# Optimization experiments

Hardware: AMD Instinct MI355X
Metric: run time of the kernel (lower is better)

Reference implementation:

```python
import jax, jax.numpy as jnp
import numpy as np

# B=batch, T=time, H=hidden_size, D=vocos_dim, I=intermediate_dim, L=num_layers,
# CB=codebook_size, CD=codebook_dim (factorized VQ)
B, T, H, D, I, L, CB, CD = 8, 2048, 1024, 384, 2048, 12, 8192, 8


def _ln(h, g, b, eps=1e-6):
    # torch LayerNorm over last dim (biased variance)
    m = h.mean(-1, keepdims=True)
    v = h.var(-1, keepdims=True)
    return (h - m) / jnp.sqrt(v + eps) * g + b


def _conv1d(x, w, b, groups=1):
    # x: (B, Cin, T), w: (Cout, Cin//groups, 7), same-pad k=7
    y = jax.lax.conv_general_dilated(
        x, w, window_strides=(1,), padding=[(3, 3)],
        dimension_numbers=('NCH', 'OIH', 'NCH'), feature_group_count=groups)
    return y + b[None, :, None]


def setup_inputs() -> dict:
    key = jax.random.key(0)
    ks = iter(jax.random.split(key, 32))
    def nrm(shape):
        return jax.random.normal(next(ks), shape, jnp.float32) * 0.02
    d = {}
    d['x'] = jax.random.normal(next(ks), (B, T, H), jnp.float32)
    # VocosBackbone (encoder): embed conv + LN + 12 ConvNeXt blocks + final LN
    d['enc_embed_w'] = nrm((D, H, 7)); d['enc_embed_b'] = jnp.zeros((D,), jnp.float32)
    d['enc_norm_g'] = jnp.ones((D,), jnp.float32); d['enc_norm_b'] = jnp.zeros((D,), jnp.float32)
    d['enc_dw_w'] = nrm((L, D, 1, 7)); d['enc_dw_b'] = jnp.zeros((L, D), jnp.float32)
    d['enc_ln_g'] = jnp.ones((L, D), jnp.float32); d['enc_ln_b'] = jnp.zeros((L, D), jnp.float32)
    d['enc_w1'] = nrm((L, I, D)); d['enc_b1'] = jnp.zeros((L, I), jnp.float32)
    d['enc_w2'] = nrm((L, D, I)); d['enc_b2'] = jnp.zeros((L, D), jnp.float32)
    d['enc_gamma'] = jnp.full((L, D), 1.0 / L, jnp.float32)  # layer_scale init 1/num_layers
    d['enc_fnorm_g'] = jnp.ones((D,), jnp.float32); d['enc_fnorm_b'] = jnp.zeros((D,), jnp.float32)
    # nn.Linear(vocos_dim, hidden_size)
    d['enc_out_w'] = nrm((H, D)); d['enc_out_b'] = jnp.zeros((H,), jnp.float32)
    # Factorized ResidualVQ (single quantizer): 1024 -> 8, 8192-entry codebook, 8 -> 1024
    d['vq_in_w'] = nrm((CD, H)); d['vq_in_b'] = jnp.zeros((CD,), jnp.float32)
    d['codebook'] = jax.random.normal(next(ks), (CB, CD), jnp.float32)
    d['vq_out_w'] = nrm((H, CD)); d['vq_out_b'] = jnp.zeros((H,), jnp.float32)
    return d


def _encode(x, ew, eb, ng, nb, dww, dwb, lng, lnb, w1, b1, w2, b2, gamma, fg, fb, ow, ob):
    # x: (B, T, H) -> encoder output (B, T, H)
    h = _conv1d(x.transpose(0, 2, 1), ew, eb)            # (B, D, T)
    h = _ln(h.transpose(0, 2, 1), ng, nb)                # (B, T, D)
    for i in range(L):
        res = h
        y = _conv1d(h.transpose(0, 2, 1), dww[i], dwb[i], groups=D)  # depthwise (B, D, T)
        y = _ln(y.transpose(0, 2, 1), lng[i], lnb[i])                # (B, T, D)
        y = jax.nn.gelu(y @ w1[i].T + b1[i], approximate=False)       # (B, T, I)
        y = (y @ w2[i].T + b2[i]) * gamma[i]                          # (B, T, D)
        h = res + y
    h = _ln(h, fg, fb)
    return h @ ow.T + ob                                  # (B, T, H)


def _quantize(enc, in_w, in_b, codebook, out_w, out_b):
    z_e = enc @ in_w.T + in_b                             # (B, T, CD)
    z_n = z_e / jnp.maximum(jnp.linalg.norm(z_e, axis=-1, keepdims=True), 1e-12)
    cb_n = codebook / jnp.maximum(jnp.linalg.norm(codebook, axis=-1, keepdims=True), 1e-12)
    sim = jnp.einsum('btd,nd->btn', z_n, cb_n)            # cosine sim == argmin l2 on normalized vecs
    idx = jnp.argmax(sim, axis=-1)                        # (B, T) int
    z_q = codebook[idx]                                   # (B, T, CD) unnormalized codebook entries
    z_q = z_e + jax.lax.stop_gradient(z_q - z_e)          # straight-through estimator
    quantized = z_q @ out_w.T + out_b                     # (B, T, H)
    return idx, quantized


def reference(x, enc_embed_w, enc_embed_b, enc_norm_g, enc_norm_b, enc_dw_w, enc_dw_b,
              enc_ln_g, enc_ln_b, enc_w1, enc_b1, enc_w2, enc_b2, enc_gamma,
              enc_fnorm_g, enc_fnorm_b, enc_out_w, enc_out_b,
              vq_in_w, vq_in_b, codebook, vq_out_w, vq_out_b):
    enc = _encode(x, enc_embed_w, enc_embed_b, enc_norm_g, enc_norm_b, enc_dw_w, enc_dw_b,
                  enc_ln_g, enc_ln_b, enc_w1, enc_b1, enc_w2, enc_b2, enc_gamma,
                  enc_fnorm_g, enc_fnorm_b, enc_out_w, enc_out_b)
    idx, quantized = _quantize(enc, vq_in_w, vq_in_b, codebook, vq_out_w, vq_out_b)
    # RepCodec.quantize returns (indices (B,T), quantized_out.transpose(1,2) -> (B,T,H))
    return idx, quantized
```

## Files before the change

### kernel.cpp

```cpp
#include <hip/hip_runtime.h>
#include <math.h>


typedef _Float16 h8_t __attribute__((ext_vector_type(8)));
typedef _Float16 h4_t __attribute__((ext_vector_type(4)));
typedef float f4_t __attribute__((ext_vector_type(4)));

__device__ __forceinline__ float gelu_exact(float x){
  return 0.5f * x * (1.0f + erff(x * 0.70710678118654752f));
}

__device__ __forceinline__ void split4(const float4& a, h4_t& hi, h4_t& lo){
  float f[4] = {a.x,a.y,a.z,a.w};
  #pragma unroll
  for (int t=0;t<4;t++){
    _Float16 hh = (_Float16)f[t];
    hi[t] = hh;
    lo[t] = (_Float16)(f[t] - (float)hh);
  }
}

__device__ __forceinline__ int swz(int row, int kg){
  return row*32 + ((kg ^ ((row>>1)&3))<<3);
}

__device__ __forceinline__ void xcd_remap(int& bx, int& by){
  const int gx = gridDim.x;
  const int nwg = gx * gridDim.y;
  int bid = by*gx + bx;
  if ((nwg & 7) == 0){
    bid = (bid & 7)*(nwg >> 3) + (bid >> 3);
    bx = bid % gx; by = bid / gx;
  }
}


__global__ __launch_bounds__(256) void prep_wk_split(const float* __restrict__ w,
                                                     _Float16* __restrict__ wh,
                                                     _Float16* __restrict__ wl){
  int i = blockIdx.x*256 + threadIdx.x;
  if (i >= 384*1024) return;
  int d = i >> 10, c = i & 1023;
  #pragma unroll
  for (int k=0;k<7;k++){
    float v = w[(size_t)d*(1024*7) + (size_t)c*7 + k];
    _Float16 hh = (_Float16)v;
    wh[(size_t)k*393216 + i] = hh;
    wl[(size_t)k*393216 + i] = (_Float16)(v - (float)hh);
  }
}

__global__ __launch_bounds__(256) void prep_cb(const float* __restrict__ cb, float* __restrict__ cbn){
  int e = blockIdx.x*256 + threadIdx.x;
  if (e >= 8192) return;
  float v[8], s = 0.f;
  #pragma unroll
  for (int cd=0; cd<8; ++cd){ v[cd] = cb[(size_t)e*8+cd]; s += v[cd]*v[cd]; }
  float inv = 1.0f / fmaxf(sqrtf(s), 1e-12f);
  #pragma unroll
  for (int cd=0; cd<8; ++cd) cbn[(size_t)e*8+cd] = v[cd]*inv;
}

__global__ __launch_bounds__(256) void prep_cw(const float* __restrict__ viw, const float* __restrict__ ow,
                                               const float* __restrict__ vib, const float* __restrict__ ob,
                                               float* __restrict__ cw, float* __restrict__ cbias){
  int i = blockIdx.x*256 + threadIdx.x;
  if (i < 3072){
    int c = i / 384, d = i - c*384;
    float acc = 0.f;
    for (int h=0; h<1024; ++h)
      acc = fmaf(viw[c*1024+h], ow[(size_t)h*384 + d], acc);
    cw[i] = acc;
  }
  if (blockIdx.x == 0 && threadIdx.x < 8){
    int c = threadIdx.x;
    float acc = vib[c];
    for (int h=0; h<1024; ++h) acc = fmaf(viw[c*1024+h], ob[h], acc);
    cbias[c] = acc;
  }
}

__global__ __launch_bounds__(256) void split_pair(const float* __restrict__ a, const float* __restrict__ b,
                                                  _Float16* __restrict__ ah, _Float16* __restrict__ al,
                                                  _Float16* __restrict__ bh, _Float16* __restrict__ bl,
                                                  int n4){
  int i = blockIdx.x*256 + threadIdx.x;
  if (i >= n4) return;
  h4_t hi, lo;
  float4 va = ((const float4*)a)[i];
  split4(va, hi, lo);
  ((h4_t*)ah)[i] = hi; ((h4_t*)al)[i] = lo;
  float4 vb = ((const float4*)b)[i];
  split4(vb, hi, lo);
  ((h4_t*)bh)[i] = hi; ((h4_t*)bl)[i] = lo;
}

__global__ __launch_bounds__(256) void split_one(const float* __restrict__ a,
                                                 _Float16* __restrict__ ah, _Float16* __restrict__ al,
                                                 int n4){
  int i = blockIdx.x*256 + threadIdx.x;
  if (i >= n4) return;
  h4_t hi, lo;
  float4 va = ((const float4*)a)[i];
  split4(va, hi, lo);
  ((h4_t*)ah)[i] = hi; ((h4_t*)al)[i] = lo;
}

template<int BN, int EPI>
__global__ __launch_bounds__(256,2) void gemm_s(
    const _Float16* __restrict__ Ah, const _Float16* __restrict__ Al, int lda,
    const _Float16* __restrict__ Bh, const _Float16* __restrict__ Bl, int ldb,
    const float* __restrict__ bias,
    _Float16* __restrict__ Ch, _Float16* __restrict__ Cl,
    int ldc, int K)
{
  constexpr int NF = BN/32;
  __shared__ _Float16 AsH[4096], AsL[4096];
  __shared__ _Float16 BsH[BN*32], BsL[BN*32];
  const int tid = threadIdx.x;
  int bx = blockIdx.x, by = blockIdx.y;
  xcd_remap(bx, by);
  const int m0 = by*128, n0 = bx*BN;
  const int srow = tid>>2, kgs = tid&3, koff = kgs*8;
  const _Float16* pAh = Ah + (size_t)(m0+srow)*lda + koff;
  const _Float16* pAl = Al + (size_t)(m0+srow)*lda + koff;
  const _Float16* pBh = Bh + (size_t)(n0+srow)*ldb + koff;
  const _Float16* pBl = Bl + (size_t)(n0+srow)*ldb + koff;
  const int sA0 = swz(srow, kgs), sA1 = swz(srow+64, kgs);
  const int lane = tid & 63, wid = tid >> 6;
  const int wm = (wid>>1)*64, wn = (wid&1)*(BN/2);
  const int fr = lane & 15, kg = lane >> 4;
  f4_t acc[4][NF] = {};
  h8_t rah0 = *(const h8_t*)(pAh);
  h8_t rah1 = *(const h8_t*)(pAh + (size_t)64*lda);
  h8_t ral0 = *(const h8_t*)(pAl);
  h8_t ral1 = *(const h8_t*)(pAl + (size_t)64*lda);
  h8_t rbh0 = *(const h8_t*)(pBh);
  h8_t rbl0 = *(const h8_t*)(pBl);
  h8_t rbh1, rbl1;
  if constexpr (BN == 128){
    rbh1 = *(const h8_t*)(pBh + (size_t)64*ldb);
    rbl1 = *(const h8_t*)(pBl + (size_t)64*ldb);
  }
  for (int k0 = 0; k0 < K; k0 += 32){
    __syncthreads();
    *(h8_t*)(AsH + sA0) = rah0; *(h8_t*)(AsL + sA0) = ral0;
    *(h8_t*)(AsH + sA1) = rah1; *(h8_t*)(AsL + sA1) = ral1;
    *(h8_t*)(BsH + sA0) = rbh0; *(h8_t*)(BsL + sA0) = rbl0;
    if constexpr (BN == 128){
      *(h8_t*)(BsH + sA1) = rbh1; *(h8_t*)(BsL + sA1) = rbl1;
    }
    if (k0 + 32 < K){
      const int kn = k0 + 32;
      rah0 = *(const h8_t*)(pAh + kn);
      rah1 = *(const h8_t*)(pAh + (size_t)64*lda + kn);
      ral0 = *(const h8_t*)(pAl + kn);
      ral1 = *(const h8_t*)(pAl + (size_t)64*lda + kn);
      rbh0 = *(const h8_t*)(pBh + kn);
      rbl0 = *(const h8_t*)(pBl + kn);
      if constexpr (BN == 128){
        rbh1 = *(const h8_t*)(pBh + (size_t)64*ldb + kn);
        rbl1 = *(const h8_t*)(pBl + (size_t)64*ldb + kn);
      }
    }
    __syncthreads();
    h8_t ah[4], al[4], bh[NF], bl[NF];
    #pragma unroll
    for (int m=0;m<4;m++){
      int o = swz(wm + fr + m*16, kg);
      ah[m] = *(const h8_t*)(AsH + o);
      al[m] = *(const h8_t*)(AsL + o);
    }
    #pragma unroll
    for (int n=0;n<NF;n++){
      int o = swz(wn + fr + n*16, kg);
      bh[n] = *(const h8_t*)(BsH + o);
      bl[n] = *(const h8_t*)(BsL + o);
    }
    __builtin_amdgcn_s_setprio(1);
    #pragma unroll
    for (int m=0;m<4;m++)
      #pragma unroll
      for (int n=0;n<NF;n++){
        acc[m][n] = __builtin_amdgcn_mfma_f32_16x16x32_f16(al[m], bh[n], acc[m][n], 0,0,0);
        acc[m][n] = __builtin_amdgcn_mfma_f32_16x16x32_f16(ah[m], bl[n], acc[m][n], 0,0,0);
        acc[m][n] = __builtin_amdgcn_mfma_f32_16x16x32_f16(ah[m], bh[n], acc[m][n], 0,0,0);
      }
    __builtin_amdgcn_s_setprio(0);
  }
  float bj[NF];
  #pragma unroll
  for (int n=0;n<NF;n++) bj[n] = bias ? bias[n0 + wn + n*16 + fr] : 0.0f;
  #pragma unroll
  for (int m=0;m<4;m++){
    #pragma unroll
    for (int r=0;r<4;r++){
      const int row = m0 + wm + m*16 + kg*4 + r;
      #pragma unroll
      for (int n=0;n<NF;n++){
        const int col = n0 + wn + n*16 + fr;
        float v = acc[m][n][r] + bj[n];
        if (EPI==1) v = gelu_exact(v);
        _Float16 hh = (_Float16)v;
        Ch[(size_t)row*ldc + col] = hh;
        Cl[(size_t)row*ldc + col] = (_Float16)(v - (float)hh);
      }
    }
  }
}

__global__ __launch_bounds__(256,2) void gemm64(
    const _Float16* __restrict__ Ah, const _Float16* __restrict__ Al, int lda,
    const _Float16* __restrict__ Bh, const _Float16* __restrict__ Bl, int ldb,
    const float* __restrict__ bias, const float* __restrict__ gamma,
    float* __restrict__ C, int ldc, int K)
{
  __shared__ _Float16 AsH[8192], AsL[8192];
  __shared__ _Float16 BsH[4096], BsL[4096];
  const int tid = threadIdx.x;
  int bx = blockIdx.x, by = blockIdx.y;
  xcd_remap(bx, by);
  const int m0 = by*128, n0 = bx*64;
  const int srowA = tid>>1, khA = tid&1;
  const int srowB = tid>>2, kgB = tid&3;
  const _Float16* pAh = Ah + (size_t)(m0+srowA)*lda + khA*32;
  const _Float16* pAl = Al + (size_t)(m0+srowA)*lda + khA*32;
  const _Float16* pBh = Bh + (size_t)(n0+srowB)*ldb + kgB*8;
  const _Float16* pBl = Bl + (size_t)(n0+srowB)*ldb + kgB*8;
  const int lane = tid & 63, wid = tid >> 6;
  const int wm = (wid>>1)*64, wn = (wid&1)*32;
  const int fr = lane & 15, kg = lane >> 4;
  f4_t acc[4][2] = {};
  h8_t rAh[4], rAl[4], rBh[2], rBl[2];
  auto gload = [&](int k0){
    #pragma unroll
    for (int j=0;j<4;j++){
      rAh[j] = *(const h8_t*)(pAh + k0 + j*8);
      rAl[j] = *(const h8_t*)(pAl + k0 + j*8);
    }
    #pragma unroll
    for (int t=0;t<2;t++){
      rBh[t] = *(const h8_t*)(pBh + k0 + t*32);
      rBl[t] = *(const h8_t*)(pBl + k0 + t*32);
    }
  };
  gload(0);
  const int nt = K >> 6;
  for (int it = 0; it < nt; ++it){
    __syncthreads();
    #pragma unroll
    for (int j=0;j<4;j++){
      int slot = khA*4096 + swz(srowA, j);
      *(h8_t*)(AsH + slot) = rAh[j];
      *(h8_t*)(AsL + slot) = rAl[j];
    }
    #pragma unroll
    for (int t=0;t<2;t++){
      int slot = t*2048 + swz(srowB, kgB);
      *(h8_t*)(BsH + slot) = rBh[t];
      *(h8_t*)(BsL + slot) = rBl[t];
    }
    if (it + 1 < nt) gload((it+1) << 6);
    __syncthreads();
    #pragma unroll
    for (int s=0;s<2;s++){
      h8_t ah[4], al[4], bh[2], bl[2];
      #pragma unroll
      for (int m=0;m<4;m++){
        int o = s*4096 + swz(wm + fr + m*16, kg);
        ah[m] = *(const h8_t*)(AsH + o);
        al[m] = *(const h8_t*)(AsL + o);
      }
      #pragma unroll
      for (int n=0;n<2;n++){
        int o = s*2048 + swz(wn + fr + n*16, kg);
        bh[n] = *(const h8_t*)(BsH + o);
        bl[n] = *(const h8_t*)(BsL + o);
      }
      __builtin_amdgcn_s_setprio(1);
      #pragma unroll
      for (int m=0;m<4;m++)
        #pragma unroll
        for (int n=0;n<2;n++){
          acc[m][n] = __builtin_amdgcn_mfma_f32_16x16x32_f16(al[m], bh[n], acc[m][n], 0,0,0);
          acc[m][n] = __builtin_amdgcn_mfma_f32_16x16x32_f16(ah[m], bl[n], acc[m][n], 0,0,0);
          acc[m][n] = __builtin_amdgcn_mfma_f32_16x16x32_f16(ah[m], bh[n], acc[m][n], 0,0,0);
        }
      __builtin_amdgcn_s_setprio(0);
    }
  }
  float bj[2], gj[2];
  #pragma unroll
  for (int n=0;n<2;n++){
    int col = n0 + wn + n*16 + fr;
    bj[n] = bias ? bias[col] : 0.0f;
    gj[n] = gamma[col];
  }
  #pragma unroll
  for (int m=0;m<4;m++){
    #pragma unroll
    for (int r=0;r<4;r++){
      const int row = m0 + wm + m*16 + kg*4 + r;
      #pragma unroll
      for (int n=0;n<2;n++){
        const int col = n0 + wn + n*16 + fr;
        C[(size_t)row*ldc + col] += gj[n]*(acc[m][n][r] + bj[n]);
      }
    }
  }
}

__global__ __launch_bounds__(256,2) void embed_f16(
    const _Float16* __restrict__ xh, const _Float16* __restrict__ xl,
    const _Float16* __restrict__ wkh, const _Float16* __restrict__ wkl,
    const float* __restrict__ bias, float* __restrict__ C)
{
  __shared__ _Float16 AsH[8192], AsL[8192], BsH[4096], BsL[4096];
  const int tid = threadIdx.x;
  int bx = blockIdx.x, by = blockIdx.y;
  xcd_remap(bx, by);
  const int m0 = by*128, n0 = bx*64;
  const int srowA = tid>>1, khA = tid&1;
  const int srowB = tid>>2, kgB = tid&3;
  const int rA = m0 + srowA, tA = rA & 2047;
  const int lane = tid & 63, wid = tid >> 6;
  const int wm = (wid>>1)*64, wn = (wid&1)*32;
  const int fr = lane & 15, kg = lane >> 4;
  f4_t acc[4][2] = {};
  const h8_t zero8 = {0,0,0,0,0,0,0,0};
  h8_t rAh[4], rAl[4], rBh[2], rBl[2];
  auto load_tile = [&](int it){
    const int k = it >> 4;
    const int k0 = (it & 15) << 6;
    const bool v = (unsigned)(tA + k - 3) < 2048u;
    const _Float16* ph = xh + (size_t)(rA + k - 3)*1024 + k0 + khA*32;
    const _Float16* pl = xl + (size_t)(rA + k - 3)*1024 + k0 + khA*32;
    #pragma unroll
    for (int j=0;j<4;j++){
      rAh[j] = v ? *(const h8_t*)(ph + j*8) : zero8;
      rAl[j] = v ? *(const h8_t*)(pl + j*8) : zero8;
    }
    const _Float16* qh = wkh + (size_t)k*393216 + (size_t)(n0+srowB)*1024 + k0 + kgB*8;
    const _Float16* ql = wkl + (size_t)k*393216 + (size_t)(n0+srowB)*1024 + k0 + kgB*8;
    #pragma unroll
    for (int t=0;t<2;t++){
      rBh[t] = *(const h8_t*)(qh + t*32);
      rBl[t] = *(const h8_t*)(ql + t*32);
    }
  };
  load_tile(0);
  for (int it = 0; it < 112; ++it){
    __syncthreads();
    #pragma unroll
    for (int j=0;j<4;j++){
      int slot = khA*4096 + swz(srowA, j);
      *(h8_t*)(AsH + slot) = rAh[j];
      *(h8_t*)(AsL + slot) = rAl[j];
    }
    #pragma unroll
    for (int t=0;t<2;t++){
      int slot = t*2048 + swz(srowB, kgB);
      *(h8_t*)(BsH + slot) = rBh[t];
      *(h8_t*)(BsL + slot) = rBl[t];
    }
    if (it + 1 < 112) load_tile(it + 1);
    __syncthreads();
    #pragma unroll
    for (int s=0;s<2;s++){
      h8_t ah[4], al[4], bh[2], bl[2];
      #pragma unroll
      for (int m=0;m<4;m++){
        int o = s*4096 + swz(wm + fr + m*16, kg);
        ah[m] = *(const h8_t*)(AsH + o);
        al[m] = *(const h8_t*)(AsL + o);
      }
      #pragma unroll
      for (int n=0;n<2;n++){
        int o = s*2048 + swz(wn + fr + n*16, kg);
        bh[n] = *(const h8_t*)(BsH + o);
        bl[n] = *(const h8_t*)(BsL + o);
      }
      __builtin_amdgcn_s_setprio(1);
      #pragma unroll
      for (int m=0;m<4;m++)
        #pragma unroll
        for (int n=0;n<2;n++){
          acc[m][n] = __builtin_amdgcn_mfma_f32_16x16x32_f16(al[m], bh[n], acc[m][n], 0,0,0);
          acc[m][n] = __builtin_amdgcn_mfma_f32_16x16x32_f16(ah[m], bl[n], acc[m][n], 0,0,0);
          acc[m][n] = __builtin_amdgcn_mfma_f32_16x16x32_f16(ah[m], bh[n], acc[m][n], 0,0,0);
        }
      __builtin_amdgcn_s_setprio(0);
    }
  }
  #pragma unroll
  for (int m=0;m<4;m++){
    #pragma unroll
    for (int r=0;r<4;r++){
      const int row = m0 + wm + m*16 + kg*4 + r;
      #pragma unroll
      for (int n=0;n<2;n++){
        const int col = n0 + wn + n*16 + fr;
        C[(size_t)row*384 + col] = acc[m][n][r] + bias[col];
      }
    }
  }
}

template<bool CONV, bool SPLIT>
__global__ __launch_bounds__(384) void ln_kernel(
    const float* __restrict__ in,
    const float* __restrict__ dw, const float* __restrict__ db,
    const float* __restrict__ g, const float* __restrict__ b,
    float* __restrict__ out, _Float16* __restrict__ oh, _Float16* __restrict__ ol)
{
  __shared__ float rs[6], rs2[6], stat[2];
  const int m = blockIdx.x, d = threadIdx.x;
  float v;
  if (CONV){
    const int t = m & 2047;
    float a = db[d];
    #pragma unroll
    for (int k=0;k<7;k++){
      int tt = t + k - 3;
      if ((unsigned)tt < 2048u) a = fmaf(in[(size_t)(m + k - 3)*384 + d], dw[d*7 + k], a);
    }
    v = a;
  } else {
    v = in[(size_t)m*384 + d];
  }
  float s = v, s2 = v*v;
  #pragma unroll
  for (int o=1;o<64;o<<=1){ s += __shfl_xor(s,o); s2 += __shfl_xor(s2,o); }
  const int wid = d >> 6, lane = d & 63;
  if (lane == 0){ rs[wid]=s; rs2[wid]=s2; }
  __syncthreads();
  if (d == 0){
    float S=0.f, S2=0.f;
    #pragma unroll
    for (int w=0;w<6;w++){ S+=rs[w]; S2+=rs2[w]; }
    float mean = S*(1.0f/384.0f);
    float var = fmaxf(S2*(1.0f/384.0f) - mean*mean, 0.0f);
    stat[0]=mean; stat[1]=1.0f/sqrtf(var + 1e-6f);
  }
  __syncthreads();
  float o = (v - stat[0])*stat[1]*g[d] + b[d];
  if (SPLIT){
    _Float16 hh = (_Float16)o;
    oh[(size_t)m*384 + d] = hh;
    ol[(size_t)m*384 + d] = (_Float16)(o - (float)hh);
  } else {
    out[(size_t)m*384 + d] = o;
  }
}


__global__ __launch_bounds__(256) void vq_ze(
    const float* __restrict__ y, const float* __restrict__ cw,
    const float* __restrict__ cbias, float* __restrict__ zn)
{
  __shared__ float scw[3072];
  const int tid = threadIdx.x;
  for (int i = tid; i < 3072; i += 256) scw[i] = cw[i];
  __syncthreads();
  const int wid = tid >> 6, lane = tid & 63;
  const size_t m = (size_t)blockIdx.x*4 + wid;
  float acc[8] = {};
  #pragma unroll
  for (int j=0;j<6;j++){
    float v = y[m*384 + j*64 + lane];
    #pragma unroll
    for (int cd=0;cd<8;cd++) acc[cd] = fmaf(v, scw[cd*384 + j*64 + lane], acc[cd]);
  }
  #pragma unroll
  for (int cd=0;cd<8;cd++)
    #pragma unroll
    for (int o=1;o<64;o<<=1) acc[cd] += __shfl_xor(acc[cd], o);
  if (lane == 0){
    float z[8], s = 0.f;
    #pragma unroll
    for (int cd=0;cd<8;cd++){ z[cd] = acc[cd] + cbias[cd]; s += z[cd]*z[cd]; }
    float inv = 1.0f / fmaxf(sqrtf(s), 1e-12f);
    #pragma unroll
    for (int cd=0;cd<8;cd++) zn[m*8+cd] = z[cd]*inv;
  }
}

__global__ __launch_bounds__(256) void vq_argmax(
    const float* __restrict__ zn, const float* __restrict__ cbn,
    int* __restrict__ idx_out, float* __restrict__ idx_f)
{
  __shared__ float sbest[256];
  __shared__ int   sidx[256];
  const int tid = threadIdx.x;
  const int tok = tid & 31, ch = tid >> 5;
  const size_t m = (size_t)blockIdx.x*32 + tok;
  float4 z0 = *(const float4*)&zn[m*8];
  float4 z1 = *(const float4*)&zn[m*8+4];
  float best = -1e30f; int bidx = 0;
  const float* cp = cbn + (size_t)ch*8192;
  #pragma unroll 4
  for (int e = 0; e < 1024; ++e){
    const float4 ca  = *(const float4*)&cp[e*8];
    const float4 cb4 = *(const float4*)&cp[e*8+4];
    float s = z0.x*ca.x + z0.y*ca.y + z0.z*ca.z + z0.w*ca.w
            + z1.x*cb4.x + z1.y*cb4.y + z1.z*cb4.z + z1.w*cb4.w;
    if (s > best){ best = s; bidx = ch*1024 + e; }
  }
  sbest[tid] = best; sidx[tid] = bidx;
  __syncthreads();
  if (tid < 32){
    float b = sbest[tid]; int bi = sidx[tid];
    #pragma unroll
    for (int c=1;c<8;c++){
      float ob = sbest[c*32 + tid];
      if (ob > b){ b = ob; bi = sidx[c*32 + tid]; }
    }
    idx_out[(size_t)blockIdx.x*32 + tid] = bi;
    idx_f [(size_t)blockIdx.x*32 + tid] = (float)bi;
  }
}

__global__ __launch_bounds__(256) void vq_out_kernel(
    const int* __restrict__ idx, const float* __restrict__ cb,
    const float* __restrict__ wo, const float* __restrict__ bo,
    float* __restrict__ outq)
{
  __shared__ float wT[8][1024];
  __shared__ float cbs[16][8];
  __shared__ int idxs[16];
  const int tid = threadIdx.x;
  #pragma unroll
  for (int j=0;j<4;j++){
    int hcol = j*256 + tid;
    float4 w0 = *(const float4*)&wo[(size_t)hcol*8];
    float4 w1 = *(const float4*)&wo[(size_t)hcol*8+4];
    wT[0][hcol]=w0.x; wT[1][hcol]=w0.y; wT[2][hcol]=w0.z; wT[3][hcol]=w0.w;
    wT[4][hcol]=w1.x; wT[5][hcol]=w1.y; wT[6][hcol]=w1.z; wT[7][hcol]=w1.w;
  }
  if (tid < 16) idxs[tid] = idx[blockIdx.x*16 + tid];
  __syncthreads();
  if (tid < 128){ int tk = tid>>3, cd = tid&7; cbs[tk][cd] = cb[(size_t)idxs[tk]*8 + cd]; }
  __syncthreads();
  float bb[4];
  #pragma unroll
  for (int j=0;j<4;j++) bb[j] = bo[j*256+tid];
  for (int tk=0;tk<16;tk++){
    const size_t m = (size_t)blockIdx.x*16 + tk;
    float c0=cbs[tk][0], c1=cbs[tk][1], c2=cbs[tk][2], c3=cbs[tk][3];
    float c4=cbs[tk][4], c5=cbs[tk][5], c6=cbs[tk][6], c7=cbs[tk][7];
    #pragma unroll
    for (int j=0;j<4;j++){
      int hcol = j*256 + tid;
      float v = bb[j];
      v = fmaf(c0, wT[0][hcol], v); v = fmaf(c1, wT[1][hcol], v);
      v = fmaf(c2, wT[2][hcol], v); v = fmaf(c3, wT[3][hcol], v);
      v = fmaf(c4, wT[4][hcol], v); v = fmaf(c5, wT[5][hcol], v);
      v = fmaf(c6, wT[6][hcol], v); v = fmaf(c7, wT[7][hcol], v);
      outq[m*1024 + hcol] = v;
    }
  }
}


extern "C" void kernel_launch(void* const* d_in, const int* in_sizes, int n_in,
                              void* d_out, int out_size, void* d_ws, size_t ws_size,
                              hipStream_t stream) {
  (void)in_sizes; (void)n_in; (void)out_size; (void)ws_size;
  const float* x   = (const float*)d_in[0];
  const float* eww = (const float*)d_in[1];
  const float* ewb = (const float*)d_in[2];
  const float* ng  = (const float*)d_in[3];
  const float* nb  = (const float*)d_in[4];
  const float* dww = (const float*)d_in[5];
  const float* dwb = (const float*)d_in[6];
  const float* lng = (const float*)d_in[7];
  const float* lnb = (const float*)d_in[8];
  const float* w1  = (const float*)d_in[9];
  const float* b1  = (const float*)d_in[10];
  const float* w2  = (const float*)d_in[11];
  const float* b2  = (const float*)d_in[12];
  const float* gma = (const float*)d_in[13];
  const float* fg  = (const float*)d_in[14];
  const float* fb  = (const float*)d_in[15];
  const float* ow  = (const float*)d_in[16];
  const float* ob  = (const float*)d_in[17];
  const float* viw = (const float*)d_in[18];
  const float* vib = (const float*)d_in[19];
  const float* cb  = (const float*)d_in[20];
  const float* vow = (const float*)d_in[21];
  const float* vob = (const float*)d_in[22];
  float* out = (float*)d_out;

  float* ws = (float*)d_ws;
  float* wreg = ws;
  _Float16* wkh = (_Float16*)wreg;
  _Float16* wkl = wkh + 2752512;
  _Float16* w1h = (_Float16*)wreg;
  _Float16* w1l = w1h + 786432;
  _Float16* w2h = w1h + 1572864;
  _Float16* w2l = w1h + 2359296;
  float* zn  = wreg + 1048576;
  float* cbn = wreg + 1179648;
  int*  idxb = (int*)(wreg + 1245184);
  float* cw  = wreg + 1261568;
  float* cbias = wreg + 1264640;
  float* h   = ws + 2752512;
  float* ylreg = ws + 9043968;
  float* yf32 = ylreg;
  _Float16* ylh = (_Float16*)ylreg;
  _Float16* yll = ylh + 6291456;
  float* y1reg = ws + 15335424;
  _Float16* xh  = (_Float16*)y1reg;
  _Float16* xl  = xh + 16777216;
  _Float16* y1h = (_Float16*)y1reg;
  _Float16* y1l = y1h + 16777216;

  prep_wk_split<<<dim3(1536), dim3(256), 0, stream>>>(eww, wkh, wkl);
  split_one<<<dim3(16384), dim3(256), 0, stream>>>(x, xh, xl, 4194304);
  embed_f16<<<dim3(6,128), dim3(256), 0, stream>>>(xh, xl, wkh, wkl, ewb, yf32);
  ln_kernel<false,false><<<dim3(16384), dim3(384), 0, stream>>>(
      yf32, nullptr, nullptr, ng, nb, h, nullptr, nullptr);

  for (int i = 0; i < 12; ++i){
    split_pair<<<dim3(768), dim3(256), 0, stream>>>(
        w1 + (size_t)i*786432, w2 + (size_t)i*786432, w1h, w1l, w2h, w2l, 196608);
    ln_kernel<true,true><<<dim3(16384), dim3(384), 0, stream>>>(
        h, dww + (size_t)i*2688, dwb + (size_t)i*384,
        lng + (size_t)i*384, lnb + (size_t)i*384, nullptr, ylh, yll);
    for (int ic = 0; ic < 2; ++ic){
      gemm_s<128,1><<<dim3(8,128), dim3(256), 0, stream>>>(
          ylh, yll, 384,
          w1h + (size_t)ic*393216, w1l + (size_t)ic*393216, 384,
          b1 + (size_t)i*2048 + (size_t)ic*1024,
          y1h, y1l, 1024, 384);
      gemm64<<<dim3(6,128), dim3(256), 0, stream>>>(
          y1h, y1l, 1024,
          w2h + (size_t)ic*1024, w2l + (size_t)ic*1024, 2048,
          (ic == 0) ? (b2 + (size_t)i*384) : nullptr,
          gma + (size_t)i*384,
          h, 384, 1024);
    }
  }

  ln_kernel<false,false><<<dim3(16384), dim3(384), 0, stream>>>(
      h, nullptr, nullptr, fg, fb, yf32, nullptr, nullptr);
  prep_cw<<<dim3(12), dim3(256), 0, stream>>>(viw, ow, vib, ob, cw, cbias);
  prep_cb<<<dim3(32), dim3(256), 0, stream>>>(cb, cbn);
  vq_ze<<<dim3(4096), dim3(256), 0, stream>>>(yf32, cw, cbias, zn);
  vq_argmax<<<dim3(512), dim3(256), 0, stream>>>(zn, cbn, idxb, out);
  vq_out_kernel<<<dim3(1024), dim3(256), 0, stream>>>(idxb, cb, vow, vob, out + 16384);
}
```

Baseline: 3.761 ms.

## Use 256x128 tiles with 32x32 MFMA for FFN up-projection, shrink K-tile elsewhere

The first FFN GEMM (w1 plus GELU) now uses 256x128 block tiles and 32x32x16 MFMA instructions, so fewer blocks each reuse more data per LDS load. The down-projection and embed-conv GEMMs drop from a 64-wide K step to a 32-wide K step, which halves their LDS footprint to allow higher occupancy but doubles the number of barrier-separated iterations. The larger w1 tile raises register and LDS pressure, and the B-tile store in gemm_n64 needs a conditional offset for rows beyond 64.

```diff
diff --git a/kernel.cpp b/kernel.cpp
--- a/kernel.cpp
+++ b/kernel.cpp
@@ -5,6 +5,7 @@
 typedef _Float16 h8_t __attribute__((ext_vector_type(8)));
 typedef _Float16 h4_t __attribute__((ext_vector_type(4)));
 typedef float f4_t __attribute__((ext_vector_type(4)));
+typedef float f32x16 __attribute__((ext_vector_type(16)));
 
 __device__ __forceinline__ float gelu_exact(float x){
   return 0.5f * x * (1.0f + erff(x * 0.70710678118654752f));
@@ -106,21 +107,123 @@
   ((h4_t*)ah)[i] = hi; ((h4_t*)al)[i] = lo;
 }
 
-template<int BN, int EPI>
-__global__ __launch_bounds__(256,2) void gemm_s(
+__global__ __launch_bounds__(256,2) void gemm_w2(
     const _Float16* __restrict__ Ah, const _Float16* __restrict__ Al, int lda,
     const _Float16* __restrict__ Bh, const _Float16* __restrict__ Bl, int ldb,
     const float* __restrict__ bias,
     _Float16* __restrict__ Ch, _Float16* __restrict__ Cl,
     int ldc, int K)
 {
-  constexpr int NF = BN/32;
-  __shared__ _Float16 AsH[4096], AsL[4096];
-  __shared__ _Float16 BsH[BN*32], BsL[BN*32];
+  __shared__ _Float16 AsH[8192], AsL[8192];
+  __shared__ _Float16 BsH[4096], BsL[4096];
   const int tid = threadIdx.x;
   int bx = blockIdx.x, by = blockIdx.y;
   xcd_remap(bx, by);
-  const int m0 = by*128, n0 = bx*BN;
+  const int m0 = by*256, n0 = bx*128;
+  const int srow = tid>>2, kgs = tid&3, koff = kgs*8;
+  const _Float16* pAh = Ah + (size_t)(m0+srow)*lda + koff;
+  const _Float16* pAl = Al + (size_t)(m0+srow)*lda + koff;
+  const _Float16* pBh = Bh + (size_t)(n0+srow)*ldb + koff;
+  const _Float16* pBl = Bl + (size_t)(n0+srow)*ldb + koff;
+  int sA[4], sB[2];
+  #pragma unroll
+  for (int r=0;r<4;r++) sA[r] = swz(srow + r*64, kgs);
+  #pragma unroll
+  for (int r=0;r<2;r++) sB[r] = swz(srow + r*64, kgs);
+  const int lane = tid & 63, wid = tid >> 6;
+  const int wm = (wid>>1)*128, wn = (wid&1)*64;
+  const int rl = lane & 31, ks2 = lane >> 5;
+  f32x16 acc[4][2] = {};
+  h8_t rAh[4], rAl[4], rBh[2], rBl[2];
+  auto gload = [&](int t){
+    const int kn = t << 5;
+    #pragma unroll
+    for (int r=0;r<4;r++){
+      rAh[r] = *(const h8_t*)(pAh + (size_t)(r*64)*lda + kn);
+      rAl[r] = *(const h8_t*)(pAl + (size_t)(r*64)*lda + kn);
+    }
+    #pragma unroll
+    for (int r=0;r<2;r++){
+      rBh[r] = *(const h8_t*)(pBh + (size_t)(r*64)*ldb + kn);
+      rBl[r] = *(const h8_t*)(pBl + (size_t)(r*64)*ldb + kn);
+    }
+  };
+  gload(0);
+  const int nt = K >> 5;
+  for (int t = 0; t < nt; ++t){
+    __syncthreads();
+    #pragma unroll
+    for (int r=0;r<4;r++){
+      *(h8_t*)(AsH + sA[r]) = rAh[r];
+      *(h8_t*)(AsL + sA[r]) = rAl[r];
+    }
+    #pragma unroll
+    for (int r=0;r<2;r++){
+      *(h8_t*)(BsH + sB[r]) = rBh[r];
+      *(h8_t*)(BsL + sB[r]) = rBl[r];
+    }
+    if (t + 1 < nt) gload(t+1);
+    __syncthreads();
+    #pragma unroll
+    for (int kk=0; kk<2; kk++){
+      h8_t ah[4], al[4], bh[2], bl[2];
+      const int kgf = kk*2 + ks2;
+      #pragma unroll
+      for (int m=0;m<4;m++){
+        int o = swz(wm + m*32 + rl, kgf);
+        ah[m] = *(const h8_t*)(AsH + o);
+        al[m] = *(const h8_t*)(AsL + o);
+      }
+      #pragma unroll
+      for (int n=0;n<2;n++){
+        int o = swz(wn + n*32 + rl, kgf);
+        bh[n] = *(const h8_t*)(BsH + o);
+        bl[n] = *(const h8_t*)(BsL + o);
+      }
+      __builtin_amdgcn_s_setprio(1);
+      #pragma unroll
+      for (int m=0;m<4;m++)
+        #pragma unroll
+        for (int n=0;n<2;n++){
+          acc[m][n] = __builtin_amdgcn_mfma_f32_32x32x16_f16(al[m], bh[n], acc[m][n], 0,0,0);
+          acc[m][n] = __builtin_amdgcn_mfma_f32_32x32x16_f16(ah[m], bl[n], acc[m][n], 0,0,0);
+          acc[m][n] = __builtin_amdgcn_mfma_f32_32x32x16_f16(ah[m], bh[n], acc[m][n], 0,0,0);
+        }
+      __builtin_amdgcn_s_setprio(0);
+    }
+  }
+  float bj[2];
+  #pragma unroll
+  for (int n=0;n<2;n++) bj[n] = bias ? bias[n0 + wn + n*32 + rl] : 0.0f;
+  #pragma unroll
+  for (int m=0;m<4;m++){
+    #pragma unroll
+    for (int n=0;n<2;n++){
+      const int col = n0 + wn + n*32 + rl;
+      #pragma unroll
+      for (int reg=0; reg<16; reg++){
+        const int row = m0 + wm + m*32 + (reg&3) + 8*(reg>>2) + 4*ks2;
+        float v = gelu_exact(acc[m][n][reg] + bj[n]);
+        _Float16 hh = (_Float16)v;
+        Ch[(size_t)row*ldc + col] = hh;
+        Cl[(size_t)row*ldc + col] = (_Float16)(v - (float)hh);
+      }
+    }
+  }
+}
+
+__global__ __launch_bounds__(256,2) void gemm_n64(
+    const _Float16* __restrict__ Ah, const _Float16* __restrict__ Al, int lda,
+    const _Float16* __restrict__ Bh, const _Float16* __restrict__ Bl, int ldb,
+    const float* __restrict__ bias, const float* __restrict__ gamma,
+    float* __restrict__ C, int ldc, int K)
+{
+  __shared__ _Float16 AsH[4096], AsL[4096];
+  __shared__ _Float16 BsH[2048], BsL[2048];
+  const int tid = threadIdx.x;
+  int bx = blockIdx.x, by = blockIdx.y;
+  xcd_remap(bx, by);
+  const int m0 = by*128, n0 = bx*64;
   const int srow = tid>>2, kgs = tid&3, koff = kgs*8;
   const _Float16* pAh = Ah + (size_t)(m0+srow)*lda + koff;
   const _Float16* pAl = Al + (size_t)(m0+srow)*lda + koff;
@@ -128,28 +231,21 @@
   const _Float16* pBl = Bl + (size_t)(n0+srow)*ldb + koff;
   const int sA0 = swz(srow, kgs), sA1 = swz(srow+64, kgs);
   const int lane = tid & 63, wid = tid >> 6;
-  const int wm = (wid>>1)*64, wn = (wid&1)*(BN/2);
+  const int wm = (wid>>1)*64, wn = (wid&1)*32;
   const int fr = lane & 15, kg = lane >> 4;
-  f4_t acc[4][NF] = {};
+  f4_t acc[4][2] = {};
   h8_t rah0 = *(const h8_t*)(pAh);
   h8_t rah1 = *(const h8_t*)(pAh + (size_t)64*lda);
   h8_t ral0 = *(const h8_t*)(pAl);
   h8_t ral1 = *(const h8_t*)(pAl + (size_t)64*lda);
   h8_t rbh0 = *(const h8_t*)(pBh);
   h8_t rbl0 = *(const h8_t*)(pBl);
-  h8_t rbh1, rbl1;
-  if constexpr (BN == 128){
-    rbh1 = *(const h8_t*)(pBh + (size_t)64*ldb);
-    rbl1 = *(const h8_t*)(pBl + (size_t)64*ldb);
-  }
   for (int k0 = 0; k0 < K; k0 += 32){
     __syncthreads();
     *(h8_t*)(AsH + sA0) = rah0; *(h8_t*)(AsL + sA0) = ral0;
     *(h8_t*)(AsH + sA1) = rah1; *(h8_t*)(AsL + sA1) = ral1;
-    *(h8_t*)(BsH + sA0) = rbh0; *(h8_t*)(BsL + sA0) = rbl0;
-    if constexpr (BN == 128){
-      *(h8_t*)(BsH + sA1) = rbh1; *(h8_t*)(BsL + sA1) = rbl1;
-    }
+    if (srow < 64){ *(h8_t*)(BsH + sA0) = rbh0; *(h8_t*)(BsL + sA0) = rbl0; }
+    else          { *(h8_t*)(BsH + sA1 - 2048) = rbh0; *(h8_t*)(BsL + sA1 - 2048) = rbl0; }
     if (k0 + 32 < K){
       const int kn = k0 + 32;
       rah0 = *(const h8_t*)(pAh + kn);
@@ -158,13 +254,9 @@
       ral1 = *(const h8_t*)(pAl + (size_t)64*lda + kn);
       rbh0 = *(const h8_t*)(pBh + kn);
       rbl0 = *(const h8_t*)(pBl + kn);
-      if constexpr (BN == 128){
-        rbh1 = *(const h8_t*)(pBh + (size_t)64*ldb + kn);
-        rbl1 = *(const h8_t*)(pBl + (size_t)64*ldb + kn);
-      }
     }
     __syncthreads();
-    h8_t ah[4], al[4], bh[NF], bl[NF];
+    h8_t ah[4], al[4], bh[2], bl[2];
     #pragma unroll
     for (int m=0;m<4;m++){
       int o = swz(wm + fr + m*16, kg);
@@ -172,7 +264,7 @@
       al[m] = *(const h8_t*)(AsL + o);
     }
     #pragma unroll
-    for (int n=0;n<NF;n++){
+    for (int n=0;n<2;n++){
       int o = swz(wn + fr + n*16, kg);
       bh[n] = *(const h8_t*)(BsH + o);
       bl[n] = *(const h8_t*)(BsL + o);
@@ -181,114 +273,13 @@
     #pragma unroll
     for (int m=0;m<4;m++)
       #pragma unroll
-      for (int n=0;n<NF;n++){
+      for (int n=0;n<2;n++){
         acc[m][n] = __builtin_amdgcn_mfma_f32_16x16x32_f16(al[m], bh[n], acc[m][n], 0,0,0);
         acc[m][n] = __builtin_amdgcn_mfma_f32_16x16x32_f16(ah[m], bl[n], acc[m][n], 0,0,0);
         acc[m][n] = __builtin_amdgcn_mfma_f32_16x16x32_f16(ah[m], bh[n], acc[m][n], 0,0,0);
       }
     __builtin_amdgcn_s_setprio(0);
   }
-  float bj[NF];
-  #pragma unroll
-  for (int n=0;n<NF;n++) bj[n] = bias ? bias[n0 + wn + n*16 + fr] : 0.0f;
-  #pragma unroll
-  for (int m=0;m<4;m++){
-    #pragma unroll
-    for (int r=0;r<4;r++){
-      const int row = m0 + wm + m*16 + kg*4 + r;
-      #pragma unroll
-      for (int n=0;n<NF;n++){
-        const int col = n0 + wn + n*16 + fr;
-        float v = acc[m][n][r] + bj[n];
-        if (EPI==1) v = gelu_exact(v);
-        _Float16 hh = (_Float16)v;
-        Ch[(size_t)row*ldc + col] = hh;
-        Cl[(size_t)row*ldc + col] = (_Float16)(v - (float)hh);
-      }
-    }
-  }
-}
-
-__global__ __launch_bounds__(256,2) void gemm64(
-    const _Float16* __restrict__ Ah, const _Float16* __restrict__ Al, int lda,
-    const _Float16* __restrict__ Bh, const _Float16* __restrict__ Bl, int ldb,
-    const float* __restrict__ bias, const float* __restrict__ gamma,
-    float* __restrict__ C, int ldc, int K)
-{
-  __shared__ _Float16 AsH[8192], AsL[8192];
-  __shared__ _Float16 BsH[4096], BsL[4096];
-  const int tid = threadIdx.x;
-  int bx = blockIdx.x, by = blockIdx.y;
-  xcd_remap(bx, by);
-  const int m0 = by*128, n0 = bx*64;
-  const int srowA = tid>>1, khA = tid&1;
-  const int srowB = tid>>2, kgB = tid&3;
-  const _Float16* pAh = Ah + (size_t)(m0+srowA)*lda + khA*32;
-  const _Float16* pAl = Al + (size_t)(m0+srowA)*lda + khA*32;
-  const _Float16* pBh = Bh + (size_t)(n0+srowB)*ldb + kgB*8;
-  const _Float16* pBl = Bl + (size_t)(n0+srowB)*ldb + kgB*8;
-  const int lane = tid & 63, wid = tid >> 6;
-  const int wm = (wid>>1)*64, wn = (wid&1)*32;
-  const int fr = lane & 15, kg = lane >> 4;
-  f4_t acc[4][2] = {};
-  h8_t rAh[4], rAl[4], rBh[2], rBl[2];
-  auto gload = [&](int k0){
-    #pragma unroll
-    for (int j=0;j<4;j++){
-      rAh[j] = *(const h8_t*)(pAh + k0 + j*8);
-      rAl[j] = *(const h8_t*)(pAl + k0 + j*8);
-    }
-    #pragma unroll
-    for (int t=0;t<2;t++){
-      rBh[t] = *(const h8_t*)(pBh + k0 + t*32);
-      rBl[t] = *(const h8_t*)(pBl + k0 + t*32);
-    }
-  };
-  gload(0);
-  const int nt = K >> 6;
-  for (int it = 0; it < nt; ++it){
-    __syncthreads();
-    #pragma unroll
-    for (int j=0;j<4;j++){
-      int slot = khA*4096 + swz(srowA, j);
-      *(h8_t*)(AsH + slot) = rAh[j];
-      *(h8_t*)(AsL + slot) = rAl[j];
-    }
-    #pragma unroll
-    for (int t=0;t<2;t++){
-      int slot = t*2048 + swz(srowB, kgB);
-      *(h8_t*)(BsH + slot) = rBh[t];
-      *(h8_t*)(BsL + slot) = rBl[t];
-    }
-    if (it + 1 < nt) gload((it+1) << 6);
-    __syncthreads();
-    #pragma unroll
-    for (int s=0;s<2;s++){
-      h8_t ah[4], al[4], bh[2], bl[2];
-      #pragma unroll
-      for (int m=0;m<4;m++){
-        int o = s*4096 + swz(wm + fr + m*16, kg);
-        ah[m] = *(const h8_t*)(AsH + o);
-        al[m] = *(const h8_t*)(AsL + o);
-      }
-      #pragma unroll
-      for (int n=0;n<2;n++){
-        int o = s*2048 + swz(wn + fr + n*16, kg);
-        bh[n] = *(const h8_t*)(BsH + o);
-        bl[n] = *(const h8_t*)(BsL + o);
-      }
-      __builtin_amdgcn_s_setprio(1);
-      #pragma unroll
-      for (int m=0;m<4;m++)
-        #pragma unroll
-        for (int n=0;n<2;n++){
-          acc[m][n] = __builtin_amdgcn_mfma_f32_16x16x32_f16(al[m], bh[n], acc[m][n], 0,0,0);
-          acc[m][n] = __builtin_amdgcn_mfma_f32_16x16x32_f16(ah[m], bl[n], acc[m][n], 0,0,0);
-          acc[m][n] = __builtin_amdgcn_mfma_f32_16x16x32_f16(ah[m], bh[n], acc[m][n], 0,0,0);
-        }
-      __builtin_amdgcn_s_setprio(0);
-    }
-  }
   float bj[2], gj[2];
   #pragma unroll
   for (int n=0;n<2;n++){
@@ -315,82 +306,70 @@
     const _Float16* __restrict__ wkh, const _Float16* __restrict__ wkl,
     const float* __restrict__ bias, float* __restrict__ C)
 {
-  __shared__ _Float16 AsH[8192], AsL[8192], BsH[4096], BsL[4096];
+  __shared__ _Float16 AsH[4096], AsL[4096], BsH[2048], BsL[2048];
   const int tid = threadIdx.x;
   int bx = blockIdx.x, by = blockIdx.y;
   xcd_remap(bx, by);
   const int m0 = by*128, n0 = bx*64;
-  const int srowA = tid>>1, khA = tid&1;
-  const int srowB = tid>>2, kgB = tid&3;
-  const int rA = m0 + srowA, tA = rA & 2047;
+  const int srow = tid>>2, kgs = tid&3, koff = kgs*8;
+  const int sA0 = swz(srow, kgs), sA1 = swz(srow+64, kgs);
   const int lane = tid & 63, wid = tid >> 6;
   const int wm = (wid>>1)*64, wn = (wid&1)*32;
   const int fr = lane & 15, kg = lane >> 4;
+  const int r0 = m0 + srow, r1 = r0 + 64;
+  const int t0 = r0 & 2047, t1 = r1 & 2047;
   f4_t acc[4][2] = {};
   const h8_t zero8 = {0,0,0,0,0,0,0,0};
-  h8_t rAh[4], rAl[4], rBh[2], rBl[2];
-  auto load_tile = [&](int it){
-    const int k = it >> 4;
-    const int k0 = (it & 15) << 6;
-    const bool v = (unsigned)(tA + k - 3) < 2048u;
-    const _Float16* ph = xh + (size_t)(rA + k - 3)*1024 + k0 + khA*32;
-    const _Float16* pl = xl + (size_t)(rA + k - 3)*1024 + k0 + khA*32;
-    #pragma unroll
-    for (int j=0;j<4;j++){
-      rAh[j] = v ? *(const h8_t*)(ph + j*8) : zero8;
-      rAl[j] = v ? *(const h8_t*)(pl + j*8) : zero8;
-    }
-    const _Float16* qh = wkh + (size_t)k*393216 + (size_t)(n0+srowB)*1024 + k0 + kgB*8;
-    const _Float16* ql = wkl + (size_t)k*393216 + (size_t)(n0+srowB)*1024 + k0 + kgB*8;
-    #pragma unroll
-    for (int t=0;t<2;t++){
-      rBh[t] = *(const h8_t*)(qh + t*32);
-      rBl[t] = *(const h8_t*)(ql + t*32);
-    }
+  h8_t rah0, rah1, ral0, ral1, rbh0, rbl0;
+  auto load_tile = [&](int kt){
+    const int k = kt >> 5;
+    const int k0 = (kt & 31) << 5;
+    const bool v0 = (unsigned)(t0 + k - 3) < 2048u;
+    const bool v1 = (unsigned)(t1 + k - 3) < 2048u;
+    rah0 = zero8; rah1 = zero8; ral0 = zero8; ral1 = zero8;
+    if (v0){
+      const size_t o = (size_t)(r0 + k - 3)*1024 + k0 + koff;
+      rah0 = *(const h8_t*)(xh + o); ral0 = *(const h8_t*)(xl + o);
+    }
+    if (v1){
+      const size_t o = (size_t)(r1 + k - 3)*1024 + k0 + koff;
+      rah1 = *(const h8_t*)(xh + o); ral1 = *(const h8_t*)(xl + o);
+    }
+    const size_t wo = (size_t)k*393216 + (size_t)(n0+srow)*1024 + k0 + koff;
+    rbh0 = *(const h8_t*)(wkh + wo); rbl0 = *(const h8_t*)(wkl + wo);
   };
   load_tile(0);
-  for (int it = 0; it < 112; ++it){
+  for (int kt = 0; kt < 224; ++kt){
     __syncthreads();
-    #pragma unroll
-    for (int j=0;j<4;j++){
-      int slot = khA*4096 + swz(srowA, j);
-      *(h8_t*)(AsH + slot) = rAh[j];
-      *(h8_t*)(AsL + slot) = rAl[j];
-    }
-    #pragma unroll
-    for (int t=0;t<2;t++){
-      int slot = t*2048 + swz(srowB, kgB);
-      *(h8_t*)(BsH + slot) = rBh[t];
-      *(h8_t*)(BsL + slot) = rBl[t];
-    }
-    if (it + 1 < 112) load_tile(it + 1);
+    *(h8_t*)(AsH+sA0) = rah0; *(h8_t*)(AsL+sA0) = ral0;
+    *(h8_t*)(AsH+sA1) = rah1; *(h8_t*)(AsL+sA1) = ral1;
+    *(h8_t*)(BsH+sA0) = rbh0; *(h8_t*)(BsL+sA0) = rbl0;
+    if (kt + 1 < 224)
+      load_tile(kt+1);
     __syncthreads();
-    #pragma unroll
-    for (int s=0;s<2;s++){
-      h8_t ah[4], al[4], bh[2], bl[2];
-      #pragma unroll
-      for (int m=0;m<4;m++){
-        int o = s*4096 + swz(wm + fr + m*16, kg);
-        ah[m] = *(const h8_t*)(AsH + o);
-        al[m] = *(const h8_t*)(AsL + o);
+    h8_t ah[4], al[4], bh[2], bl[2];
+    #pragma unroll
+    for (int m=0;m<4;m++){
+      int o = swz(wm + fr + m*16, kg);
+      ah[m] = *(const h8_t*)(AsH + o);
+      al[m] = *(const h8_t*)(AsL + o);
+    }
+    #pragma unroll
+    for (int n=0;n<2;n++){
+      int o = swz(wn + fr + n*16, kg);
+      bh[n] = *(const h8_t*)(BsH + o);
+      bl[n] = *(const h8_t*)(BsL + o);
+    }
+    __builtin_amdgcn_s_setprio(1);
+    #pragma unroll
+    for (int m=0;m<4;m++)
+      #pragma unroll
+      for (int n=0;n<2;n++){
+        acc[m][n] = __builtin_amdgcn_mfma_f32_16x16x32_f16(al[m], bh[n], acc[m][n], 0,0,0);
+        acc[m][n] = __builtin_amdgcn_mfma_f32_16x16x32_f16(ah[m], bl[n], acc[m][n], 0,0,0);
+        acc[m][n] = __builtin_amdgcn_mfma_f32_16x16x32_f16(ah[m], bh[n], acc[m][n], 0,0,0);
       }
-      #pragma unroll
-      for (int n=0;n<2;n++){
-        int o = s*2048 + swz(wn + fr + n*16, kg);
-        bh[n] = *(const h8_t*)(BsH + o);
-        bl[n] = *(const h8_t*)(BsL + o);
-      }
-      __builtin_amdgcn_s_setprio(1);
-      #pragma unroll
-      for (int m=0;m<4;m++)
-        #pragma unroll
-        for (int n=0;n<2;n++){
-          acc[m][n] = __builtin_amdgcn_mfma_f32_16x16x32_f16(al[m], bh[n], acc[m][n], 0,0,0);
-          acc[m][n] = __builtin_amdgcn_mfma_f32_16x16x32_f16(ah[m], bl[n], acc[m][n], 0,0,0);
-          acc[m][n] = __builtin_amdgcn_mfma_f32_16x16x32_f16(ah[m], bh[n], acc[m][n], 0,0,0);
-        }
-      __builtin_amdgcn_s_setprio(0);
-    }
+    __builtin_amdgcn_s_setprio(0);
   }
   #pragma unroll
   for (int m=0;m<4;m++){
@@ -628,12 +607,12 @@
         h, dww + (size_t)i*2688, dwb + (size_t)i*384,
         lng + (size_t)i*384, lnb + (size_t)i*384, nullptr, ylh, yll);
     for (int ic = 0; ic < 2; ++ic){
-      gemm_s<128,1><<<dim3(8,128), dim3(256), 0, stream>>>(
+      gemm_w2<<<dim3(8,64), dim3(256), 0, stream>>>(
           ylh, yll, 384,
           w1h + (size_t)ic*393216, w1l + (size_t)ic*393216, 384,
           b1 + (size_t)i*2048 + (size_t)ic*1024,
           y1h, y1l, 1024, 384);
-      gemm64<<<dim3(6,128), dim3(256), 0, stream>>>(
+      gemm_n64<<<dim3(6,128), dim3(256), 0, stream>>>(
           y1h, y1l, 1024,
           w2h + (size_t)ic*1024, w2l + (size_t)ic*1024, 2048,
           (ic == 0) ? (b2 + (size_t)i*384) : nullptr,
```

Result: slower. 4.060 ms (+8.0%).
